# Kernel optimization log

Measured on AMD Instinct MI355X. Metric: run time of the kernel, lower is better.

## Reference

```python
import jax, jax.numpy as jnp
import numpy as np

N = 100000
E = 1600000
D_IN = 128
D_HID = 32
NEG_SLOPE = 0.2


def _glorot(key, shape):
    fan_in, fan_out = shape[0], shape[-1]
    lim = jnp.sqrt(6.0 / (fan_in + fan_out))
    return jax.random.uniform(key, shape, jnp.float32, -lim, lim)


def setup_inputs() -> dict:
    key = jax.random.key(0)
    ks = jax.random.split(key, 10)
    x = jax.random.normal(ks[0], (N, D_IN), jnp.float32)
    edge_index = jax.random.randint(ks[1], (2, E), 0, N, jnp.int64)
    return {
        "x": x,
        "edge_index": edge_index,
        "W1_l": _glorot(ks[2], (D_IN, D_HID)),
        "W1_r": _glorot(ks[3], (D_IN, D_HID)),
        "att1": _glorot(ks[4], (D_HID,)),
        "b1": jnp.zeros((D_HID,), jnp.float32),
        "W2_l": _glorot(ks[5], (D_HID, D_HID)),
        "W2_r": _glorot(ks[6], (D_HID, D_HID)),
        "att2": _glorot(ks[7], (D_HID,)),
        "b2": jnp.zeros((D_HID,), jnp.float32),
    }


def _segment_softmax(logits, seg, num_segments):
    m = jax.ops.segment_max(logits, seg, num_segments=num_segments)
    m = jnp.where(jnp.isfinite(m), m, 0.0)
    ex = jnp.exp(logits - m[seg])
    s = jax.ops.segment_sum(ex, seg, num_segments=num_segments)
    return ex / (s[seg] + 1e-16)


def _gatv2(x, edge_index, W_l, W_r, att, b):
    # GATv2Conv, heads=1, add_self_loops=False, share_weights=False
    src, dst = edge_index[0], edge_index[1]
    x_l = x @ W_l  # source transform [N, D_HID]
    x_r = x @ W_r  # target transform [N, D_HID]
    # per-edge attention logit: att . leaky_relu(x_l[j] + x_r[i])
    h = x_l[src] + x_r[dst]  # [E, D_HID]
    e = jnp.where(h > 0, h, NEG_SLOPE * h) @ att  # [E]
    alpha = _segment_softmax(e, dst, x.shape[0])  # softmax over incoming edges
    out = jax.ops.segment_sum(alpha[:, None] * x_l[src], dst,
                              num_segments=x.shape[0])
    return out + b


def reference(x, edge_index, W1_l, W1_r, att1, b1, W2_l, W2_r, att2, b2):
    h = _gatv2(x, edge_index, W1_l, W1_r, att1, b1)
    h = jax.nn.relu(h)
    return _gatv2(h, edge_index, W2_l, W2_r, att2, b2)
```

## Files before the change

### kernel.cpp

```cpp
#include <hip/hip_runtime.h>
#include <hip/hip_bf16.h>

#define D_HID 32
#define D_IN 128
#define NEG 0.2f
#define BSH 7
#define BSZ 128
#define MAXB 1024
#define CAP  4096
#define NSCAT 1024

typedef unsigned short u16;
typedef __attribute__((ext_vector_type(8))) short short8;
typedef __attribute__((ext_vector_type(4))) float float4v;

__device__ __forceinline__ float b2f(u16 u){
  union { unsigned int i; float f; } c; c.i = ((unsigned int)u) << 16; return c.f;
}

__device__ __forceinline__ u16 f2b_rne(float f){
  union { float f; unsigned int u; } c; c.f = f;
  unsigned int u = c.u;
  return (u16)((u + 0x7FFFu + ((u >> 16) & 1u)) >> 16);
}

__device__ __forceinline__ void split_bf16(float v, u16& hi, u16& lo){
  hi = f2b_rne(v);
  lo = f2b_rne(v - b2f(hi));
}

__device__ __forceinline__ float ldf(const void* __restrict__ p, int f32, long long i){
  return f32 ? ((const float*)p)[i] : b2f(((const u16*)p)[i]);
}

__device__ __forceinline__ int atomAddI(int* p, int v){
  return __hip_atomic_fetch_add(p, v, __ATOMIC_RELAXED, __HIP_MEMORY_SCOPE_AGENT);
}

__device__ __forceinline__ float red8(float p){
  p += __int_as_float(__builtin_amdgcn_update_dpp(
         0, __float_as_int(p), 0xB1, 0xF, 0xF, true));
  p += __int_as_float(__builtin_amdgcn_update_dpp(
         0, __float_as_int(p), 0x4E, 0xF, 0xF, true));
  p += __int_as_float(__builtin_amdgcn_ds_swizzle(
         __float_as_int(p), 0x101F));
  return p;
}

__device__ __forceinline__ float edge_ev(const float4 xv, const float4 xrk,
                                         const float4 attk){
  float hx = xv.x + xrk.x; hx = fmaxf(hx, NEG*hx);
  float hy = xv.y + xrk.y; hy = fmaxf(hy, NEG*hy);
  float hz = xv.z + xrk.z; hz = fmaxf(hz, NEG*hz);
  float hw = xv.w + xrk.w; hw = fmaxf(hw, NEG*hw);
  float p = hx*attk.x;
  p = fmaf(hy, attk.y, p);
  p = fmaf(hz, attk.z, p);
  p = fmaf(hw, attk.w, p);
  p = red8(p);
  p = fminf(p, 60.f);
  return __expf(p);
}

__device__ __forceinline__ void prep_body(const void* __restrict__ Wl,
                                          const void* __restrict__ Wr,
                                          int f32, int K,
                                          uint4* __restrict__ whi,
                                          uint4* __restrict__ wlo, int t){
  int KS = K >> 5;
  int total = 4 * KS * 64;
  if (t >= total) return;
  int lane = t & 63;
  int rem = t >> 6;
  int kstep = rem % KS;
  int ctile = rem / KS;
  int col = ctile * 16 + (lane & 15);
  int quad = lane >> 4;
  union { u16 s[8]; uint4 q; } ch, cl;
  #pragma unroll
  for (int j = 0; j < 8; ++j){
    int k = kstep*32 + quad*8 + j;
    float v = (col < 32) ? ldf(Wl, f32, (long long)k*D_HID + col)
                         : ldf(Wr, f32, (long long)k*D_HID + (col - 32));
    u16 hi, lo; split_bf16(v, hi, lo);
    ch.s[j] = hi; cl.s[j] = lo;
  }
  whi[rem*64 + lane] = ch.q;
  wlo[rem*64 + lane] = cl.q;
}

__global__ void __launch_bounds__(256)
scat_prep(const int* __restrict__ ei, const u16* __restrict__ xw,
          int* __restrict__ cursor, unsigned* __restrict__ seg,
          int* __restrict__ flags,
          const void* __restrict__ W1l, const void* __restrict__ W1r,
          const void* __restrict__ W2l, const void* __restrict__ W2r,
          uint4* __restrict__ whi1, uint4* __restrict__ wlo1,
          uint4* __restrict__ whi2, uint4* __restrict__ wlo2,
          int E_, int B_){
  int t = threadIdx.x;
  if ((int)blockIdx.x >= NSCAT){
    __shared__ int ins_p;
    if (t == 0) ins_p = 0;
    __syncthreads();
    int e = (xw[t] >> 7) & 0xFF;
    if (e < 100 || e > 140) atomicAdd(&ins_p, 1);
    __syncthreads();
    int f32 = (ins_p > 16) ? 1 : 0;
    int sub = blockIdx.x - NSCAT;
    if (sub < 4) prep_body(W1l, W1r, f32, D_IN,  whi1, wlo1, sub*256 + t);
    else         prep_body(W2l, W2r, f32, D_HID, whi2, wlo2, t);
    return;
  }
  __shared__ int hist[MAXB];
  __shared__ int bbase[MAXB];
  __shared__ int nz_s, insane_s;
  if (t == 0){ nz_s = 0; insane_s = 0; }
  for (int i = t; i < B_; i += 256) hist[i] = 0;
  __syncthreads();
  if (t < 64 && ei[2*t+1] != 0) atomicAdd(&nz_s, 1);
  if (blockIdx.x == 0){
    int e = (xw[t] >> 7) & 0xFF;
    if (e < 100 || e > 140) atomicAdd(&insane_s, 1);
  }
  __syncthreads();
  int is64 = (nz_s == 0);
  if (blockIdx.x == 0 && t == 0){
    flags[0] = is64;
    flags[1] = (insane_s > 16) ? 1 : 0;
  }
  int chunk = (E_ + NSCAT - 1) / NSCAT;
  int s = blockIdx.x * chunk;
  int e = s + chunk; if (e > E_) e = E_;
  for (int i = s + t; i < e; i += 256){
    int dst = is64 ? ei[2*E_ + 2*i] : ei[E_ + i];
    atomicAdd(&hist[dst >> BSH], 1);
  }
  __syncthreads();
  for (int i = t; i < B_; i += 256){
    int c = hist[i];
    bbase[i] = c ? atomAddI(&cursor[i], c) : 0;
  }
  __syncthreads();
  for (int i = t; i < B_; i += 256) hist[i] = 0;
  __syncthreads();
  for (int i = s + t; i < e; i += 256){
    int src, dst;
    if (is64){ src = ei[2*i]; dst = ei[2*E_ + 2*i]; }
    else     { src = ei[i];   dst = ei[E_ + i]; }
    int b = dst >> BSH;
    int pos = bbase[b] + atomicAdd(&hist[b], 1);
    if (pos < CAP)
      seg[(size_t)b*CAP + pos] = ((unsigned)src << BSH) | (unsigned)(dst & (BSZ-1));
  }
}

__device__ void finalize_body(const unsigned* __restrict__ seg,
                              const int* __restrict__ cursor,
                              int* __restrict__ row, int* __restrict__ csr_src,
                              int N_, int B_, int b, int t){
  __shared__ int sd[MAXB];
  __shared__ int part[256];
  __shared__ int hist[BSZ];
  __shared__ int sc[BSZ];
  __shared__ int loff[BSZ];
  for (int i = t; i < MAXB; i += 256) sd[i] = (i < B_) ? min(cursor[i], CAP) : 0;
  __syncthreads();
  int a0 = sd[4*t], a1 = sd[4*t+1], a2 = sd[4*t+2], a3 = sd[4*t+3];
  int mysum = a0 + a1 + a2 + a3;
  part[t] = mysum;
  __syncthreads();
  for (int off = 1; off < 256; off <<= 1){
    int v = (t >= off) ? part[t-off] : 0;
    __syncthreads();
    part[t] += v;
    __syncthreads();
  }
  int excl = part[t] - mysum;
  sd[4*t]   = excl;
  sd[4*t+1] = excl + a0;
  sd[4*t+2] = excl + a0 + a1;
  sd[4*t+3] = excl + a0 + a1 + a2;
  __syncthreads();
  int base_out = sd[b];
  int cnt = min(cursor[b], CAP);
  int total = part[255];
  size_t base_in = (size_t)b * CAP;

  if (t < BSZ) hist[t] = 0;
  __syncthreads();
  for (int i = t; i < cnt; i += 256)
    atomicAdd(&hist[seg[base_in + i] & (BSZ-1)], 1);
  __syncthreads();
  if (t < BSZ) sc[t] = hist[t];
  __syncthreads();
  for (int off = 1; off < BSZ; off <<= 1){
    int tmp = (t < BSZ && t >= off) ? sc[t-off] : 0;
    __syncthreads();
    if (t < BSZ) sc[t] += tmp;
    __syncthreads();
  }
  if (t < BSZ){
    int e2 = sc[t] - hist[t];
    loff[t] = e2;
    int node = b*BSZ + t;
    if (node <= N_) row[node] = base_out + e2;
  }
  if (b == B_-1 && t == 0) row[N_] = total;
  __syncthreads();
  for (int i = t; i < cnt; i += 256){
    unsigned en = seg[base_in + i];
    int dl = en & (BSZ-1);
    int pos = atomicAdd(&loff[dl], 1);
    csr_src[base_out + pos] = (int)en;
  }
}

template<int K>
__device__ __forceinline__ void gemm_body(const void* __restrict__ X,
                          const uint4* __restrict__ whi, const uint4* __restrict__ wlo,
                          const int* __restrict__ flags, int force_f32,
                          float* __restrict__ xl, float* __restrict__ xr,
                          int N_, int tile, int lane)
{
  constexpr int KS = K >> 5;
  if (tile * 16 >= N_) return;
  int quad = lane >> 4;
  int m = tile*16 + (lane & 15);
  if (m >= N_) m = N_ - 1;
  int f32 = force_f32 | flags[1];

  float4v acc[4];
  #pragma unroll
  for (int c = 0; c < 4; ++c) acc[c] = (float4v){0.f,0.f,0.f,0.f};

  #pragma unroll
  for (int ks = 0; ks < KS; ++ks){
    long long base = (long long)m * K + ks*32 + quad*8;
    float av[8];
    if (f32){
      const float4* xp = (const float4*)((const float*)X + base);
      float4 t0 = xp[0], t1 = xp[1];
      av[0]=t0.x; av[1]=t0.y; av[2]=t0.z; av[3]=t0.w;
      av[4]=t1.x; av[5]=t1.y; av[6]=t1.z; av[7]=t1.w;
    } else {
      union { uint4 q; u16 s[8]; } c8;
      c8.q = *(const uint4*)((const u16*)X + base);
      #pragma unroll
      for (int j = 0; j < 8; ++j) av[j] = b2f(c8.s[j]);
    }
    short8 ahi, alo;
    #pragma unroll
    for (int j = 0; j < 8; ++j){
      u16 hi, lo; split_bf16(av[j], hi, lo);
      ahi[j] = (short)hi; alo[j] = (short)lo;
    }
    #pragma unroll
    for (int c = 0; c < 4; ++c){
      uint4 wh = whi[(c*KS + ks)*64 + lane];
      uint4 wl = wlo[(c*KS + ks)*64 + lane];
      short8 bh = *(short8*)&wh;
      short8 bl = *(short8*)&wl;
      acc[c] = __builtin_amdgcn_mfma_f32_16x16x32_bf16(ahi, bh, acc[c], 0, 0, 0);
      acc[c] = __builtin_amdgcn_mfma_f32_16x16x32_bf16(ahi, bl, acc[c], 0, 0, 0);
      acc[c] = __builtin_amdgcn_mfma_f32_16x16x32_bf16(alo, bh, acc[c], 0, 0, 0);
    }
  }

  #pragma unroll
  for (int c = 0; c < 4; ++c){
    int col = c*16 + (lane & 15);
    float* dst = (col < 32) ? xl : xr;
    int kk = col & 31;
    #pragma unroll
    for (int r = 0; r < 4; ++r){
      int node = tile*16 + quad*4 + r;
      if (node < N_) dst[(size_t)node*D_HID + kk] = acc[c][r];
    }
  }
}

template<int K>
__global__ void __launch_bounds__(256)
fin_gemm(const unsigned* __restrict__ seg, const int* __restrict__ cursor,
         int* __restrict__ row, int* __restrict__ csr_src,
         const void* __restrict__ X,
         const uint4* __restrict__ whi, const uint4* __restrict__ wlo,
         const int* __restrict__ flags,
         float* __restrict__ xl, float* __restrict__ xr, int N_, int B_){
  if ((int)blockIdx.x < B_){
    finalize_body(seg, cursor, row, csr_src, N_, B_, blockIdx.x, threadIdx.x);
    return;
  }
  int tile = (blockIdx.x - B_) * 4 + (threadIdx.x >> 6);
  gemm_body<K>(X, whi, wlo, flags, 0, xl, xr, N_, tile, threadIdx.x & 63);
}

template<int K>
__global__ void __launch_bounds__(256)
mfma_gemm(const void* __restrict__ X,
          const uint4* __restrict__ whi, const uint4* __restrict__ wlo,
          const int* __restrict__ flags, int force_f32,
          float* __restrict__ xl, float* __restrict__ xr, int N_){
  int tile = blockIdx.x * 4 + (threadIdx.x >> 6);
  gemm_body<K>(X, whi, wlo, flags, force_f32, xl, xr, N_, tile, threadIdx.x & 63);
}

__global__ void __launch_bounds__(256)
gat_gather(const int* __restrict__ row, const unsigned* __restrict__ csrp,
           const float* __restrict__ xl, const float* __restrict__ xr,
           const void* __restrict__ att, const void* __restrict__ bias,
           const int* __restrict__ flags,
           float* __restrict__ outp, int N_, int do_relu)
{
  int wv = (blockIdx.x * blockDim.x + threadIdx.x) >> 6;
  int l = threadIdx.x & 63;
  int n = wv * 4 + (l >> 4);
  if (n >= N_) return;
  int half = (l >> 3) & 1;
  int fl = l & 7;
  int f32 = flags[1];
  float4 attk;
  attk.x = ldf(att, f32, fl*4+0);
  attk.y = ldf(att, f32, fl*4+1);
  attk.z = ldf(att, f32, fl*4+2);
  attk.w = ldf(att, f32, fl*4+3);
  float4 xrk = *(const float4*)(xr + (size_t)n*D_HID + fl*4);
  int rs = row[n], re = row[n+1];
  const char* xlb = (const char*)xl;
  unsigned fo = (unsigned)(fl << 4);

  float4 acc = make_float4(0.f, 0.f, 0.f, 0.f);
  float ssum = 0.f;

  int start = rs + 2*half;
  if (start < re){
    int last = re - 1;
    unsigned c0 = csrp[start];
    unsigned c1 = csrp[min(start+1,  last)];
    unsigned c2 = csrp[min(start+4,  last)];
    unsigned c3 = csrp[min(start+5,  last)];
    unsigned c4 = csrp[min(start+8,  last)];
    unsigned c5 = csrp[min(start+9,  last)];
    unsigned ca = csrp[min(start+12, last)];
    unsigned cb = csrp[min(start+13, last)];
    float4 xv0 = *(const float4*)(xlb + (c0 & ~127u) + fo);
    float4 xv1 = *(const float4*)(xlb + (c1 & ~127u) + fo);
    float4 xv2 = *(const float4*)(xlb + (c2 & ~127u) + fo);
    float4 xv3 = *(const float4*)(xlb + (c3 & ~127u) + fo);
    float4 xv4 = *(const float4*)(xlb + (c4 & ~127u) + fo);
    float4 xv5 = *(const float4*)(xlb + (c5 & ~127u) + fo);
    for (int i = start; i < re; i += 4){
      float4 nx0 = *(const float4*)(xlb + (ca & ~127u) + fo);
      float4 nx1 = *(const float4*)(xlb + (cb & ~127u) + fo);
      unsigned na = csrp[min(i+16, last)];
      unsigned nb = csrp[min(i+17, last)];
      float ev0 = edge_ev(xv0, xrk, attk);
      ssum += ev0;
      acc.x = fmaf(ev0, xv0.x, acc.x);
      acc.y = fmaf(ev0, xv0.y, acc.y);
      acc.z = fmaf(ev0, xv0.z, acc.z);
      acc.w = fmaf(ev0, xv0.w, acc.w);
      float ev1 = edge_ev(xv1, xrk, attk);
      ev1 = (i + 1 <= last) ? ev1 : 0.f;
      ssum += ev1;
      acc.x = fmaf(ev1, xv1.x, acc.x);
      acc.y = fmaf(ev1, xv1.y, acc.y);
      acc.z = fmaf(ev1, xv1.z, acc.z);
      acc.w = fmaf(ev1, xv1.w, acc.w);
      xv0 = xv2; xv1 = xv3; xv2 = xv4; xv3 = xv5; xv4 = nx0; xv5 = nx1;
      ca = na; cb = nb;
    }
  }

  acc.x += __shfl_xor(acc.x, 8, 16);
  acc.y += __shfl_xor(acc.y, 8, 16);
  acc.z += __shfl_xor(acc.z, 8, 16);
  acc.w += __shfl_xor(acc.w, 8, 16);
  ssum  += __shfl_xor(ssum,  8, 16);

  if (half == 0){
    float inv = 1.0f / (ssum + 1e-16f);
    float4 o;
    o.x = acc.x*inv + ldf(bias, f32, fl*4+0);
    o.y = acc.y*inv + ldf(bias, f32, fl*4+1);
    o.z = acc.z*inv + ldf(bias, f32, fl*4+2);
    o.w = acc.w*inv + ldf(bias, f32, fl*4+3);
    if (do_relu){
      o.x = fmaxf(o.x, 0.f); o.y = fmaxf(o.y, 0.f);
      o.z = fmaxf(o.z, 0.f); o.w = fmaxf(o.w, 0.f);
    }
    *(float4*)(outp + (size_t)n*D_HID + fl*4) = o;
  }
}

extern "C" void kernel_launch(void* const* d_in, const int* in_sizes, int n_in,
                              void* d_out, int out_size, void* d_ws, size_t ws_size,
                              hipStream_t stream)
{
  const void* x   = d_in[0];
  const int*  ei  = (const int*)d_in[1];
  const void* W1l = d_in[2];
  const void* W1r = d_in[3];
  const void* att1= d_in[4];
  const void* b1  = d_in[5];
  const void* W2l = d_in[6];
  const void* W2r = d_in[7];
  const void* att2= d_in[8];
  const void* b2  = d_in[9];
  float* out = (float*)d_out;

  int N_ = in_sizes[0] / D_IN;
  int E_ = in_sizes[1] / 2;
  int B_ = (N_ + BSZ - 1) / BSZ;

  char* ws = (char*)d_ws;
  size_t off = 0;
  auto carve = [&](size_t bytes) -> char* {
    char* p = ws + off;
    off += (bytes + 255) & ~(size_t)255;
    return p;
  };
  float*    xl      = (float*)   carve((size_t)N_ * D_HID * 4);
  float*    xr      = (float*)   carve((size_t)N_ * D_HID * 4);
  float*    h       = (float*)   carve((size_t)N_ * D_HID * 4);
  unsigned* seg     = (unsigned*)carve((size_t)B_ * CAP * 4);
  int*      csr_src = (int*)     carve((size_t)E_ * 4);
  int*      row     = (int*)     carve((size_t)(N_ + 1) * 4);
  int*      cursor  = (int*)     carve((size_t)MAXB * 4);
  int*      flags   = (int*)     carve(256);
  uint4*    whi1    = (uint4*)   carve((size_t)4 * 4 * 64 * 16);
  uint4*    wlo1    = (uint4*)   carve((size_t)4 * 4 * 64 * 16);
  uint4*    whi2    = (uint4*)   carve((size_t)4 * 1 * 64 * 16);
  uint4*    wlo2    = (uint4*)   carve((size_t)4 * 1 * 64 * 16);

  const int tpb = 256;
  int gG = (N_ + 15) / 16;
  int tiles = (N_ + 15) / 16;
  int gT = (tiles + 3) / 4;

  hipMemsetAsync(cursor, 0, (size_t)MAXB * 4, stream);

  scat_prep<<<NSCAT + 5, tpb, 0, stream>>>(
      ei, (const u16*)x, cursor, seg, flags,
      W1l, W1r, W2l, W2r, whi1, wlo1, whi2, wlo2, E_, B_);

  fin_gemm<D_IN><<<B_ + gT, tpb, 0, stream>>>(
      seg, cursor, row, csr_src, x, whi1, wlo1, flags, xl, xr, N_, B_);

  gat_gather<<<gG, tpb, 0, stream>>>(row, (const unsigned*)csr_src, xl, xr,
                                     att1, b1, flags, h, N_, 1);

  mfma_gemm<D_HID><<<gT, tpb, 0, stream>>>(h, whi2, wlo2, flags, 1, xl, xr, N_);

  gat_gather<<<gG, tpb, 0, stream>>>(row, (const unsigned*)csr_src, xl, xr,
                                     att2, b2, flags, out, N_, 0);
}
```

Measured before the change: 255.4 us.

## Coarsen destination buckets to 1024 nodes and use 1024-thread finalize blocks

Each destination bucket now covers 1024 nodes instead of 128, so there are about 98 buckets instead of about 782, and each bucket holds up to 20480 edges. The scatter pass does fewer global cursor atomics and smaller shared-memory histograms. The finalize pass now does a single 128-entry scan of bucket sizes, and the fused finalize/GEMM kernel runs with 1024-thread blocks. Packed CSR entries now keep 10 local-destination bits, so the gather kernels shift the entry right by 3 to get the source feature offset. In exchange there are far fewer finalize blocks, each doing a longer 1024-step scan, and large blocks may reduce occupancy flexibility for the GEMM part.

```diff
diff --git a/kernel.cpp b/kernel.cpp
--- a/kernel.cpp
+++ b/kernel.cpp
@@ -4,15 +4,17 @@
 #define D_HID 32
 #define D_IN 128
 #define NEG 0.2f
-#define BSH 7
-#define BSZ 128
-#define MAXB 1024
-#define CAP  4096
-#define NSCAT 1024
+#define BSH 10
+#define BSZ 1024
+#define MAXB 128
+#define CAP  20480
+#define NSCAT 512
 
 typedef unsigned short u16;
 typedef __attribute__((ext_vector_type(8))) short short8;
 typedef __attribute__((ext_vector_type(4))) float float4v;
+
+#define XOFF(en) (((en) >> 3) & ~127u)
 
 __device__ __forceinline__ float b2f(u16 u){
   union { unsigned int i; float f; } c; c.i = ((unsigned int)u) << 16; return c.f;
@@ -116,7 +118,7 @@
   __shared__ int bbase[MAXB];
   __shared__ int nz_s, insane_s;
   if (t == 0){ nz_s = 0; insane_s = 0; }
-  for (int i = t; i < B_; i += 256) hist[i] = 0;
+  if (t < MAXB) hist[t] = 0;
   __syncthreads();
   if (t < 64 && ei[2*t+1] != 0) atomicAdd(&nz_s, 1);
   if (blockIdx.x == 0){
@@ -137,12 +139,11 @@
     atomicAdd(&hist[dst >> BSH], 1);
   }
   __syncthreads();
-  for (int i = t; i < B_; i += 256){
-    int c = hist[i];
-    bbase[i] = c ? atomAddI(&cursor[i], c) : 0;
-  }
-  __syncthreads();
-  for (int i = t; i < B_; i += 256) hist[i] = 0;
+  if (t < MAXB){
+    int c = hist[t];
+    bbase[t] = c ? atomAddI(&cursor[t], c) : 0;
+    hist[t] = 0;
+  }
   __syncthreads();
   for (int i = s + t; i < e; i += 256){
     int src, dst;
@@ -159,56 +160,44 @@
                               const int* __restrict__ cursor,
                               int* __restrict__ row, int* __restrict__ csr_src,
                               int N_, int B_, int b, int t){
-  __shared__ int sd[MAXB];
-  __shared__ int part[256];
+  __shared__ int sd[128];
   __shared__ int hist[BSZ];
   __shared__ int sc[BSZ];
   __shared__ int loff[BSZ];
-  for (int i = t; i < MAXB; i += 256) sd[i] = (i < B_) ? min(cursor[i], CAP) : 0;
-  __syncthreads();
-  int a0 = sd[4*t], a1 = sd[4*t+1], a2 = sd[4*t+2], a3 = sd[4*t+3];
-  int mysum = a0 + a1 + a2 + a3;
-  part[t] = mysum;
-  __syncthreads();
-  for (int off = 1; off < 256; off <<= 1){
-    int v = (t >= off) ? part[t-off] : 0;
-    __syncthreads();
-    part[t] += v;
-    __syncthreads();
-  }
-  int excl = part[t] - mysum;
-  sd[4*t]   = excl;
-  sd[4*t+1] = excl + a0;
-  sd[4*t+2] = excl + a0 + a1;
-  sd[4*t+3] = excl + a0 + a1 + a2;
-  __syncthreads();
-  int base_out = sd[b];
+  if (t < 128) sd[t] = (t < B_) ? min(cursor[t], CAP) : 0;
+  hist[t] = 0;
+  __syncthreads();
+  for (int off = 1; off < 128; off <<= 1){
+    int v = (t < 128 && t >= off) ? sd[t-off] : 0;
+    __syncthreads();
+    if (t < 128) sd[t] += v;
+    __syncthreads();
+  }
   int cnt = min(cursor[b], CAP);
-  int total = part[255];
+  int base_out = sd[b] - cnt;
+  int total = sd[127];
   size_t base_in = (size_t)b * CAP;
 
-  if (t < BSZ) hist[t] = 0;
-  __syncthreads();
-  for (int i = t; i < cnt; i += 256)
+  for (int i = t; i < cnt; i += 1024)
     atomicAdd(&hist[seg[base_in + i] & (BSZ-1)], 1);
   __syncthreads();
-  if (t < BSZ) sc[t] = hist[t];
+  sc[t] = hist[t];
   __syncthreads();
   for (int off = 1; off < BSZ; off <<= 1){
-    int tmp = (t < BSZ && t >= off) ? sc[t-off] : 0;
-    __syncthreads();
-    if (t < BSZ) sc[t] += tmp;
-    __syncthreads();
-  }
-  if (t < BSZ){
-    int e2 = sc[t] - hist[t];
-    loff[t] = e2;
+    int tmp = (t >= off) ? sc[t-off] : 0;
+    __syncthreads();
+    sc[t] += tmp;
+    __syncthreads();
+  }
+  {
+    int excl = sc[t] - hist[t];
+    loff[t] = excl;
     int node = b*BSZ + t;
-    if (node <= N_) row[node] = base_out + e2;
+    if (node <= N_) row[node] = base_out + excl;
   }
   if (b == B_-1 && t == 0) row[N_] = total;
   __syncthreads();
-  for (int i = t; i < cnt; i += 256){
+  for (int i = t; i < cnt; i += 1024){
     unsigned en = seg[base_in + i];
     int dl = en & (BSZ-1);
     int pos = atomicAdd(&loff[dl], 1);
@@ -281,7 +270,7 @@
 }
 
 template<int K>
-__global__ void __launch_bounds__(256)
+__global__ void __launch_bounds__(1024)
 fin_gemm(const unsigned* __restrict__ seg, const int* __restrict__ cursor,
          int* __restrict__ row, int* __restrict__ csr_src,
          const void* __restrict__ X,
@@ -292,7 +281,7 @@
     finalize_body(seg, cursor, row, csr_src, N_, B_, blockIdx.x, threadIdx.x);
     return;
   }
-  int tile = (blockIdx.x - B_) * 4 + (threadIdx.x >> 6);
+  int tile = (blockIdx.x - B_) * 16 + (threadIdx.x >> 6);
   gemm_body<K>(X, whi, wlo, flags, 0, xl, xr, N_, tile, threadIdx.x & 63);
 }
 
@@ -344,15 +333,15 @@
     unsigned c5 = csrp[min(start+9,  last)];
     unsigned ca = csrp[min(start+12, last)];
     unsigned cb = csrp[min(start+13, last)];
-    float4 xv0 = *(const float4*)(xlb + (c0 & ~127u) + fo);
-    float4 xv1 = *(const float4*)(xlb + (c1 & ~127u) + fo);
-    float4 xv2 = *(const float4*)(xlb + (c2 & ~127u) + fo);
-    float4 xv3 = *(const float4*)(xlb + (c3 & ~127u) + fo);
-    float4 xv4 = *(const float4*)(xlb + (c4 & ~127u) + fo);
-    float4 xv5 = *(const float4*)(xlb + (c5 & ~127u) + fo);
+    float4 xv0 = *(const float4*)(xlb + XOFF(c0) + fo);
+    float4 xv1 = *(const float4*)(xlb + XOFF(c1) + fo);
+    float4 xv2 = *(const float4*)(xlb + XOFF(c2) + fo);
+    float4 xv3 = *(const float4*)(xlb + XOFF(c3) + fo);
+    float4 xv4 = *(const float4*)(xlb + XOFF(c4) + fo);
+    float4 xv5 = *(const float4*)(xlb + XOFF(c5) + fo);
     for (int i = start; i < re; i += 4){
-      float4 nx0 = *(const float4*)(xlb + (ca & ~127u) + fo);
-      float4 nx1 = *(const float4*)(xlb + (cb & ~127u) + fo);
+      float4 nx0 = *(const float4*)(xlb + XOFF(ca) + fo);
+      float4 nx1 = *(const float4*)(xlb + XOFF(cb) + fo);
       unsigned na = csrp[min(i+16, last)];
       unsigned nb = csrp[min(i+17, last)];
       float ev0 = edge_ev(xv0, xrk, attk);
@@ -437,7 +426,8 @@
   const int tpb = 256;
   int gG = (N_ + 15) / 16;
   int tiles = (N_ + 15) / 16;
-  int gT = (tiles + 3) / 4;
+  int gT1 = (tiles + 15) / 16;
+  int gT2 = (tiles + 3) / 4;
 
   hipMemsetAsync(cursor, 0, (size_t)MAXB * 4, stream);
 
@@ -445,13 +435,13 @@
       ei, (const u16*)x, cursor, seg, flags,
       W1l, W1r, W2l, W2r, whi1, wlo1, whi2, wlo2, E_, B_);
 
-  fin_gemm<D_IN><<<B_ + gT, tpb, 0, stream>>>(
+  fin_gemm<D_IN><<<B_ + gT1, 1024, 0, stream>>>(
       seg, cursor, row, csr_src, x, whi1, wlo1, flags, xl, xr, N_, B_);
 
   gat_gather<<<gG, tpb, 0, stream>>>(row, (const unsigned*)csr_src, xl, xr,
                                      att1, b1, flags, h, N_, 1);
 
-  mfma_gemm<D_HID><<<gT, tpb, 0, stream>>>(h, whi2, wlo2, flags, 1, xl, xr, N_);
+  mfma_gemm<D_HID><<<gT2, tpb, 0, stream>>>(h, whi2, wlo2, flags, 1, xl, xr, N_);
 
   gat_gather<<<gG, tpb, 0, stream>>>(row, (const unsigned*)csr_src, xl, xr,
                                      att2, b2, flags, out, N_, 0);
```

Result: faster. 235.0 us (median of 2 runs) (-8.0%).
